# Performance work log

Hardware: AMD Instinct MI355X
Metric: run time of the kernel (lower is better)

The kernel has to match this reference:

```python
import jax, jax.numpy as jnp
import numpy as np

N = 100000      # nodes
E = 3200000     # edges (avg degree 32)
F_IN = 128      # num_node_features
H = 16          # hidden dim (fixed in module)
C = 2           # num_classes


def setup_inputs() -> dict:
    key = jax.random.key(0)
    k0, k1, k2, k3 = jax.random.split(key, 4)
    x = jax.random.normal(k0, (N, F_IN), dtype=jnp.float32)
    edge_index = jax.random.randint(k1, (2, E), 0, N, dtype=jnp.int32)
    # GCNConv params: weight (in,out) + bias (out,) per layer (glorot-ish scale)
    W1 = jax.random.normal(k2, (F_IN, H), dtype=jnp.float32) * (1.0 / np.sqrt(F_IN))
    b1 = jnp.zeros((H,), jnp.float32)
    W2 = jax.random.normal(k3, (H, C), dtype=jnp.float32) * (1.0 / np.sqrt(H))
    b2 = jnp.zeros((C,), jnp.float32)
    return {"x": x, "edge_index": edge_index, "W1": W1, "b1": b1, "W2": W2, "b2": b2}


def _gcn_conv(x, W, b, src, dst, n):
    # GCNConv: h = D^{-1/2}(A+I)D^{-1/2} (x W) + b, with self-loops in src/dst
    h = x @ W                                   # [n, out]
    deg = jax.ops.segment_sum(jnp.ones_like(dst, dtype=h.dtype), dst, num_segments=n)
    dinv = jnp.where(deg > 0, jax.lax.rsqrt(deg), 0.0)
    norm = dinv[src] * dinv[dst]                # [E+n]
    msg = h[src] * norm[:, None]                # gather + scale
    out = jax.ops.segment_sum(msg, dst, num_segments=n)  # scatter-add
    return out + b


def reference(x, edge_index, W1, b1, W2, b2):
    loops = jnp.arange(N, dtype=edge_index.dtype)
    src = jnp.concatenate([edge_index[0], loops])
    dst = jnp.concatenate([edge_index[1], loops])
    h = jax.nn.relu(_gcn_conv(x, W1, b1, src, dst, N))
    # F.dropout(training=False) in eval mode is identity
    out = _gcn_conv(h, W2, b2, src, dst, N)
    return jax.nn.log_softmax(out, axis=1)
```

## Files before the change

### kernel.cpp

```cpp
#include <hip/hip_runtime.h>

#define NN 100000
#define NE 3200000
#define FIN 128
#define HD 16

#define BSH 8
#define BSPAN 256
#define NBKT 391
#define CAP 9216
#define TPB 512

#define FXS 1048576.0f
#define FXI (1.0f / 1048576.0f)

__device__ __forceinline__ float lo2f(unsigned u) {
    union { float f; unsigned i; } v; v.i = u << 16; return v.f;
}
__device__ __forceinline__ float hi2f(unsigned u) {
    union { float f; unsigned i; } v; v.i = u & 0xFFFF0000u; return v.f;
}
__device__ __forceinline__ ushort f2b(float f) {
    union { float f; unsigned u; } v; v.f = f;
    unsigned r = (v.u + 0x7FFFu + ((v.u >> 16) & 1u)) >> 16;
    return (ushort)r;
}
__device__ __forceinline__ unsigned pck(float a, float b) {
    return (unsigned)f2b(a) | ((unsigned)f2b(b) << 16);
}

__global__ __launch_bounds__(TPB) void k_scat(const int* __restrict__ src,
                                              const int* __restrict__ dst,
                                              int* __restrict__ gcnt,
                                              unsigned* __restrict__ csrb) {
    __shared__ int h[NBKT];
    __shared__ int sbuf[TPB];
    __shared__ int lcur[NBKT];
    __shared__ int gbase[NBKT];
    __shared__ unsigned ebuf[8192];
    int b = blockIdx.x, t = threadIdx.x;
    for (int i = t; i < NBKT; i += TPB) h[i] = 0;
    __syncthreads();
    int cq = b * 2048;
    const int4* s4p = (const int4*)src;
    const int4* d4p = (const int4*)dst;
    int4 sv[4], dv[4];
    #pragma unroll
    for (int j = 0; j < 4; ++j) {
        int e4 = cq + j * TPB + t;
        if (e4 < NE / 4) {
            sv[j] = s4p[e4]; dv[j] = d4p[e4];
            atomicAdd(&h[dv[j].x >> BSH], 1);
            atomicAdd(&h[dv[j].y >> BSH], 1);
            atomicAdd(&h[dv[j].z >> BSH], 1);
            atomicAdd(&h[dv[j].w >> BSH], 1);
        }
    }
    __syncthreads();
    sbuf[t] = (t < NBKT) ? h[t] : 0;
    __syncthreads();
    for (int off = 1; off < TPB; off <<= 1) {
        int v = 0;
        if (t >= off) v = sbuf[t - off];
        __syncthreads();
        if (t >= off) sbuf[t] += v;
        __syncthreads();
    }
    if (t < NBKT) {
        int c = h[t];
        int excl = sbuf[t] - c;
        lcur[t] = excl;
        int gb = t * CAP - excl;
        if (c) gb += atomicAdd(&gcnt[t], c);
        gbase[t] = gb;
    }
    __syncthreads();
    #pragma unroll
    for (int j = 0; j < 4; ++j) {
        int e4 = cq + j * TPB + t;
        if (e4 < NE / 4) {
            int bk, p;
            bk = dv[j].x >> BSH; p = atomicAdd(&lcur[bk], 1);
            ebuf[p] = (unsigned)sv[j].x | ((unsigned)(dv[j].x & (BSPAN - 1)) << 17);
            bk = dv[j].y >> BSH; p = atomicAdd(&lcur[bk], 1);
            ebuf[p] = (unsigned)sv[j].y | ((unsigned)(dv[j].y & (BSPAN - 1)) << 17);
            bk = dv[j].z >> BSH; p = atomicAdd(&lcur[bk], 1);
            ebuf[p] = (unsigned)sv[j].z | ((unsigned)(dv[j].z & (BSPAN - 1)) << 17);
            bk = dv[j].w >> BSH; p = atomicAdd(&lcur[bk], 1);
            ebuf[p] = (unsigned)sv[j].w | ((unsigned)(dv[j].w & (BSPAN - 1)) << 17);
        }
    }
    __syncthreads();
    int ecnt = NE - b * 8192; if (ecnt > 8192) ecnt = 8192;
    for (int p = t; p < ecnt; p += TPB) {
        unsigned pl = ebuf[p];
        int lo = 0, hi = NBKT;
        while (lo < hi) { int mid = (lo + hi) >> 1;
                          if (sbuf[mid] > p) hi = mid; else lo = mid + 1; }
        csrb[gbase[lo] + p] = pl;
    }
}

__global__ __launch_bounds__(TPB) void k_gemm1d(const int* __restrict__ gcnt,
                                                const unsigned int* __restrict__ csrb,
                                                const float* __restrict__ x,
                                                const float* __restrict__ W1,
                                                float* __restrict__ dinv,
                                                ushort* __restrict__ h1b) {
    __shared__ float wsm[FIN][HD];
    __shared__ int cnt[BSPAN];
    __shared__ float dvs[BSPAN];
    int b = blockIdx.x, t = threadIdx.x;
    if (t < BSPAN) cnt[t] = 0;
    for (int i = t; i < FIN * HD; i += TPB) wsm[i >> 4][i & 15] = W1[i];
    __syncthreads();
    int e0 = b * CAP, e1 = e0 + gcnt[b];
    for (int e = e0 + t; e < e1; e += TPB) atomicAdd(&cnt[csrb[e] >> 17], 1);
    __syncthreads();
    if (t < BSPAN) {
        int node = b * BSPAN + t;
        float di = rsqrtf((float)cnt[t] + 1.0f);
        dvs[t] = di;
        if (node < NN) dinv[node] = di;
    }
    __syncthreads();
    int loc = t >> 1, half = t & 1;
    int node = b * BSPAN + loc;
    if (node >= NN) return;
    int g = half * 8;
    const float4* xr = (const float4*)(x + (size_t)node * FIN);
    float a0 = 0.f, a1 = 0.f, a2 = 0.f, a3 = 0.f;
    float a4 = 0.f, a5 = 0.f, a6 = 0.f, a7 = 0.f;
    #pragma unroll
    for (int k4 = 0; k4 < FIN / 4; ++k4) {
        float4 v = xr[k4];
        #pragma unroll
        for (int kk = 0; kk < 4; ++kk) {
            float vk = (kk == 0) ? v.x : (kk == 1) ? v.y : (kk == 2) ? v.z : v.w;
            float4 w0 = *(const float4*)&wsm[k4 * 4 + kk][g];
            float4 w1 = *(const float4*)&wsm[k4 * 4 + kk][g + 4];
            a0 += vk * w0.x; a1 += vk * w0.y; a2 += vk * w0.z; a3 += vk * w0.w;
            a4 += vk * w1.x; a5 += vk * w1.y; a6 += vk * w1.z; a7 += vk * w1.w;
        }
    }
    float di = dvs[loc];
    uint4 r = {pck(a0 * di, a1 * di), pck(a2 * di, a3 * di),
               pck(a4 * di, a5 * di), pck(a6 * di, a7 * di)};
    *(uint4*)(h1b + (size_t)node * HD + g) = r;
}

__device__ __forceinline__ void scat16(int* a, uint4 u0, uint4 u1) {
    atomicAdd(a + 0,  __float2int_rn(lo2f(u0.x) * FXS));
    atomicAdd(a + 1,  __float2int_rn(hi2f(u0.x) * FXS));
    atomicAdd(a + 2,  __float2int_rn(lo2f(u0.y) * FXS));
    atomicAdd(a + 3,  __float2int_rn(hi2f(u0.y) * FXS));
    atomicAdd(a + 4,  __float2int_rn(lo2f(u0.z) * FXS));
    atomicAdd(a + 5,  __float2int_rn(hi2f(u0.z) * FXS));
    atomicAdd(a + 6,  __float2int_rn(lo2f(u0.w) * FXS));
    atomicAdd(a + 7,  __float2int_rn(hi2f(u0.w) * FXS));
    atomicAdd(a + 8,  __float2int_rn(lo2f(u1.x) * FXS));
    atomicAdd(a + 9,  __float2int_rn(hi2f(u1.x) * FXS));
    atomicAdd(a + 10, __float2int_rn(lo2f(u1.y) * FXS));
    atomicAdd(a + 11, __float2int_rn(hi2f(u1.y) * FXS));
    atomicAdd(a + 12, __float2int_rn(lo2f(u1.z) * FXS));
    atomicAdd(a + 13, __float2int_rn(hi2f(u1.z) * FXS));
    atomicAdd(a + 14, __float2int_rn(lo2f(u1.w) * FXS));
    atomicAdd(a + 15, __float2int_rn(hi2f(u1.w) * FXS));
}

__global__ __launch_bounds__(TPB) void k_aggs1(const int* __restrict__ gcnt,
                                               const unsigned int* __restrict__ csrb,
                                               const ushort* __restrict__ h1b,
                                               const float* __restrict__ dinv,
                                               const float* __restrict__ b1,
                                               const float* __restrict__ W2,
                                               float* __restrict__ g_s) {
    __shared__ int acc[BSPAN][HD + 1];
    __shared__ float w2s[HD * 2];
    __shared__ float b1s[HD];
    int b = blockIdx.x, t = threadIdx.x;
    for (int i = t; i < BSPAN * (HD + 1); i += TPB) ((int*)acc)[i] = 0;
    if (t < HD * 2) w2s[t] = W2[t];
    else if (t < HD * 3) b1s[t - HD * 2] = b1[t - HD * 2];
    __syncthreads();
    int e0 = b * CAP, e1 = e0 + gcnt[b];
    int e = e0 + t;
    for (; e + TPB < e1; e += 2 * TPB) {
        unsigned pa = csrb[e];
        unsigned pb = csrb[e + TPB];
        const uint4* ra = (const uint4*)(h1b + (size_t)(pa & 0x1FFFF) * HD);
        const uint4* rb = (const uint4*)(h1b + (size_t)(pb & 0x1FFFF) * HD);
        uint4 a0 = ra[0], a1 = ra[1];
        uint4 c0 = rb[0], c1 = rb[1];
        scat16(acc[pa >> 17], a0, a1);
        scat16(acc[pb >> 17], c0, c1);
    }
    if (e < e1) {
        unsigned p = csrb[e];
        const uint4* r = (const uint4*)(h1b + (size_t)(p & 0x1FFFF) * HD);
        uint4 u0 = r[0], u1 = r[1];
        scat16(acc[p >> 17], u0, u1);
    }
    __syncthreads();
    int loc = t >> 1, half = t & 1;
    int node = b * BSPAN + loc;
    if (node < NN) {
        float di = dinv[node];
        const uint4 sv = *(const uint4*)(h1b + (size_t)node * HD + half * 8);
        float sf[8] = {lo2f(sv.x), hi2f(sv.x), lo2f(sv.y), hi2f(sv.y),
                       lo2f(sv.z), hi2f(sv.z), lo2f(sv.w), hi2f(sv.w)};
        const int* a = acc[loc] + half * 8;
        const float* bb = b1s + half * 8;
        const float* ww = w2s + half * 16;
        float p0 = 0.f, p1 = 0.f;
        #pragma unroll
        for (int k = 0; k < 8; ++k) {
            float v = fmaxf(di * ((float)a[k] * FXI + sf[k]) + bb[k], 0.f);
            p0 += v * ww[k * 2];
            p1 += v * ww[k * 2 + 1];
        }
        p0 += __shfl_xor(p0, 1, 64);
        p1 += __shfl_xor(p1, 1, 64);
        if (half == 0) {
            float2 r = {p0 * di, p1 * di};
            *(float2*)(g_s + (size_t)node * 2) = r;
        }
    }
}

__global__ __launch_bounds__(TPB) void k_aggs2(const int* __restrict__ gcnt,
                                               const unsigned int* __restrict__ csrb,
                                               const float* __restrict__ g_s,
                                               const float* __restrict__ dinv,
                                               const float* __restrict__ b2,
                                               float* __restrict__ out) {
    __shared__ int acc[BSPAN * 3];
    int b = blockIdx.x, t = threadIdx.x;
    for (int i = t; i < BSPAN * 3; i += TPB) acc[i] = 0;
    __syncthreads();
    int e0 = b * CAP, e1 = e0 + gcnt[b];
    int e = e0 + t;
    for (; e + TPB < e1; e += 2 * TPB) {
        unsigned pa = csrb[e];
        unsigned pb = csrb[e + TPB];
        float2 va = *(const float2*)(g_s + (size_t)(pa & 0x1FFFF) * 2);
        float2 vb = *(const float2*)(g_s + (size_t)(pb & 0x1FFFF) * 2);
        int la = (pa >> 17) * 3, lb = (pb >> 17) * 3;
        atomicAdd(&acc[la],     __float2int_rn(va.x * FXS));
        atomicAdd(&acc[la + 1], __float2int_rn(va.y * FXS));
        atomicAdd(&acc[lb],     __float2int_rn(vb.x * FXS));
        atomicAdd(&acc[lb + 1], __float2int_rn(vb.y * FXS));
    }
    if (e < e1) {
        unsigned p = csrb[e];
        float2 v = *(const float2*)(g_s + (size_t)(p & 0x1FFFF) * 2);
        int l = (p >> 17) * 3;
        atomicAdd(&acc[l],     __float2int_rn(v.x * FXS));
        atomicAdd(&acc[l + 1], __float2int_rn(v.y * FXS));
    }
    __syncthreads();
    if (t < BSPAN) {
        int node = b * BSPAN + t;
        if (node < NN) {
            float di = dinv[node];
            float2 sv = *(const float2*)(g_s + (size_t)node * 2);
            float o0 = di * ((float)acc[t * 3] * FXI + sv.x) + b2[0];
            float o1 = di * ((float)acc[t * 3 + 1] * FXI + sv.y) + b2[1];
            float mx = fmaxf(o0, o1);
            float l = mx + logf(__expf(o0 - mx) + __expf(o1 - mx));
            float2 r = {o0 - l, o1 - l};
            *(float2*)(out + (size_t)node * 2) = r;
        }
    }
}

extern "C" void kernel_launch(void* const* d_in, const int* in_sizes, int n_in,
                              void* d_out, int out_size, void* d_ws, size_t ws_size,
                              hipStream_t stream) {
    const float* x   = (const float*)d_in[0];
    const int* ei    = (const int*)d_in[1];
    const int* src   = ei;
    const int* dst   = ei + NE;
    const float* W1  = (const float*)d_in[2];
    const float* b1  = (const float*)d_in[3];
    const float* W2  = (const float*)d_in[4];
    const float* b2  = (const float*)d_in[5];
    float* out = (float*)d_out;

    char* w = (char*)d_ws;
    int*   gcnt        = (int*)w;            w += NBKT * 4;
    float* dinv        = (float*)w;          w += NN * 4;
    unsigned int* csrb = (unsigned int*)w;   w += (size_t)NBKT * CAP * 4;
    ushort* h1b        = (ushort*)w;         w += (size_t)NN * HD * 2;
    float* g_s         = (float*)w;          w += NN * 2 * 4;

    hipMemsetAsync(gcnt, 0, NBKT * 4, stream);
    k_scat   <<<NBKT, TPB, 0, stream>>>(src, dst, gcnt, csrb);
    k_gemm1d <<<NBKT, TPB, 0, stream>>>(gcnt, csrb, x, W1, dinv, h1b);
    k_aggs1  <<<NBKT, TPB, 0, stream>>>(gcnt, csrb, h1b, dinv, b1, W2, g_s);
    k_aggs2  <<<NBKT, TPB, 0, stream>>>(gcnt, csrb, g_s, dinv, b2, out);
}
```

Measured before the change: 200.2 us.

## Overlap edge bucketing with X·W1 GEMM in one launch, apply dinv at gather

Merges the edge-scatter kernel and the dense x·W1 projection into one launch, with half the blocks doing each, so the memory-bound GEMM runs alongside the bucketing. Degree normalisation moves into a small separate kernel. The source-side dinv scale is now applied per edge during aggregation, and the stored features are no longer pre-scaled. The aggregation loops are unrolled to four edges per iteration to raise memory-level parallelism. The trade is an extra per-edge dinv gather and one more kernel launch.

```diff
diff --git a/kernel.cpp b/kernel.cpp
--- a/kernel.cpp
+++ b/kernel.cpp
@@ -29,148 +29,149 @@
     return (unsigned)f2b(a) | ((unsigned)f2b(b) << 16);
 }
 
-__global__ __launch_bounds__(TPB) void k_scat(const int* __restrict__ src,
-                                              const int* __restrict__ dst,
-                                              int* __restrict__ gcnt,
-                                              unsigned* __restrict__ csrb) {
-    __shared__ int h[NBKT];
-    __shared__ int sbuf[TPB];
-    __shared__ int lcur[NBKT];
-    __shared__ int gbase[NBKT];
-    __shared__ unsigned ebuf[8192];
-    int b = blockIdx.x, t = threadIdx.x;
-    for (int i = t; i < NBKT; i += TPB) h[i] = 0;
-    __syncthreads();
-    int cq = b * 2048;
-    const int4* s4p = (const int4*)src;
-    const int4* d4p = (const int4*)dst;
-    int4 sv[4], dv[4];
-    #pragma unroll
-    for (int j = 0; j < 4; ++j) {
-        int e4 = cq + j * TPB + t;
-        if (e4 < NE / 4) {
-            sv[j] = s4p[e4]; dv[j] = d4p[e4];
-            atomicAdd(&h[dv[j].x >> BSH], 1);
-            atomicAdd(&h[dv[j].y >> BSH], 1);
-            atomicAdd(&h[dv[j].z >> BSH], 1);
-            atomicAdd(&h[dv[j].w >> BSH], 1);
-        }
-    }
-    __syncthreads();
-    sbuf[t] = (t < NBKT) ? h[t] : 0;
-    __syncthreads();
-    for (int off = 1; off < TPB; off <<= 1) {
-        int v = 0;
-        if (t >= off) v = sbuf[t - off];
-        __syncthreads();
-        if (t >= off) sbuf[t] += v;
-        __syncthreads();
-    }
-    if (t < NBKT) {
-        int c = h[t];
-        int excl = sbuf[t] - c;
-        lcur[t] = excl;
-        int gb = t * CAP - excl;
-        if (c) gb += atomicAdd(&gcnt[t], c);
-        gbase[t] = gb;
-    }
-    __syncthreads();
-    #pragma unroll
-    for (int j = 0; j < 4; ++j) {
-        int e4 = cq + j * TPB + t;
-        if (e4 < NE / 4) {
-            int bk, p;
-            bk = dv[j].x >> BSH; p = atomicAdd(&lcur[bk], 1);
-            ebuf[p] = (unsigned)sv[j].x | ((unsigned)(dv[j].x & (BSPAN - 1)) << 17);
-            bk = dv[j].y >> BSH; p = atomicAdd(&lcur[bk], 1);
-            ebuf[p] = (unsigned)sv[j].y | ((unsigned)(dv[j].y & (BSPAN - 1)) << 17);
-            bk = dv[j].z >> BSH; p = atomicAdd(&lcur[bk], 1);
-            ebuf[p] = (unsigned)sv[j].z | ((unsigned)(dv[j].z & (BSPAN - 1)) << 17);
-            bk = dv[j].w >> BSH; p = atomicAdd(&lcur[bk], 1);
-            ebuf[p] = (unsigned)sv[j].w | ((unsigned)(dv[j].w & (BSPAN - 1)) << 17);
-        }
-    }
-    __syncthreads();
-    int ecnt = NE - b * 8192; if (ecnt > 8192) ecnt = 8192;
-    for (int p = t; p < ecnt; p += TPB) {
-        unsigned pl = ebuf[p];
-        int lo = 0, hi = NBKT;
-        while (lo < hi) { int mid = (lo + hi) >> 1;
-                          if (sbuf[mid] > p) hi = mid; else lo = mid + 1; }
-        csrb[gbase[lo] + p] = pl;
-    }
-}
-
-__global__ __launch_bounds__(TPB) void k_gemm1d(const int* __restrict__ gcnt,
-                                                const unsigned int* __restrict__ csrb,
-                                                const float* __restrict__ x,
-                                                const float* __restrict__ W1,
-                                                float* __restrict__ dinv,
-                                                ushort* __restrict__ h1b) {
-    __shared__ float wsm[FIN][HD];
+union FrontSM {
+    struct { int h[NBKT]; int sbuf[TPB]; int lcur[NBKT]; int gbase[NBKT];
+             unsigned ebuf[8192]; } s;
+    struct { float wsm[FIN][HD]; } g;
+};
+
+__global__ __launch_bounds__(TPB) void k_front(const int* __restrict__ src,
+                                               const int* __restrict__ dst,
+                                               const float* __restrict__ x,
+                                               const float* __restrict__ W1,
+                                               int* __restrict__ gcnt,
+                                               unsigned* __restrict__ csrb,
+                                               ushort* __restrict__ h1u) {
+    __shared__ FrontSM sm;
+    int t = threadIdx.x;
+    if (blockIdx.x < NBKT) {
+        int b = blockIdx.x;
+        for (int i = t; i < NBKT; i += TPB) sm.s.h[i] = 0;
+        __syncthreads();
+        int cq = b * 2048;
+        const int4* s4p = (const int4*)src;
+        const int4* d4p = (const int4*)dst;
+        int4 sv[4], dv[4];
+        #pragma unroll
+        for (int j = 0; j < 4; ++j) {
+            int e4 = cq + j * TPB + t;
+            if (e4 < NE / 4) {
+                sv[j] = s4p[e4]; dv[j] = d4p[e4];
+                atomicAdd(&sm.s.h[dv[j].x >> BSH], 1);
+                atomicAdd(&sm.s.h[dv[j].y >> BSH], 1);
+                atomicAdd(&sm.s.h[dv[j].z >> BSH], 1);
+                atomicAdd(&sm.s.h[dv[j].w >> BSH], 1);
+            }
+        }
+        __syncthreads();
+        sm.s.sbuf[t] = (t < NBKT) ? sm.s.h[t] : 0;
+        __syncthreads();
+        for (int off = 1; off < TPB; off <<= 1) {
+            int v = 0;
+            if (t >= off) v = sm.s.sbuf[t - off];
+            __syncthreads();
+            if (t >= off) sm.s.sbuf[t] += v;
+            __syncthreads();
+        }
+        if (t < NBKT) {
+            int c = sm.s.h[t];
+            int excl = sm.s.sbuf[t] - c;
+            sm.s.lcur[t] = excl;
+            int gb = t * CAP - excl;
+            if (c) gb += atomicAdd(&gcnt[t], c);
+            sm.s.gbase[t] = gb;
+        }
+        __syncthreads();
+        #pragma unroll
+        for (int j = 0; j < 4; ++j) {
+            int e4 = cq + j * TPB + t;
+            if (e4 < NE / 4) {
+                int bk, p;
+                bk = dv[j].x >> BSH; p = atomicAdd(&sm.s.lcur[bk], 1);
+                sm.s.ebuf[p] = (unsigned)sv[j].x | ((unsigned)(dv[j].x & (BSPAN - 1)) << 17);
+                bk = dv[j].y >> BSH; p = atomicAdd(&sm.s.lcur[bk], 1);
+                sm.s.ebuf[p] = (unsigned)sv[j].y | ((unsigned)(dv[j].y & (BSPAN - 1)) << 17);
+                bk = dv[j].z >> BSH; p = atomicAdd(&sm.s.lcur[bk], 1);
+                sm.s.ebuf[p] = (unsigned)sv[j].z | ((unsigned)(dv[j].z & (BSPAN - 1)) << 17);
+                bk = dv[j].w >> BSH; p = atomicAdd(&sm.s.lcur[bk], 1);
+                sm.s.ebuf[p] = (unsigned)sv[j].w | ((unsigned)(dv[j].w & (BSPAN - 1)) << 17);
+            }
+        }
+        __syncthreads();
+        int ecnt = NE - b * 8192; if (ecnt > 8192) ecnt = 8192;
+        for (int p = t; p < ecnt; p += TPB) {
+            unsigned pl = sm.s.ebuf[p];
+            int lo = 0, hi = NBKT;
+            while (lo < hi) { int mid = (lo + hi) >> 1;
+                              if (sm.s.sbuf[mid] > p) hi = mid; else lo = mid + 1; }
+            csrb[sm.s.gbase[lo] + p] = pl;
+        }
+    } else {
+        int b = blockIdx.x - NBKT;
+        for (int i = t; i < FIN * HD; i += TPB) sm.g.wsm[i >> 4][i & 15] = W1[i];
+        __syncthreads();
+        int loc = t >> 1, half = t & 1;
+        int node = b * BSPAN + loc;
+        if (node >= NN) return;
+        int g = half * 8;
+        const float4* xr = (const float4*)(x + (size_t)node * FIN);
+        float a0 = 0.f, a1 = 0.f, a2 = 0.f, a3 = 0.f;
+        float a4 = 0.f, a5 = 0.f, a6 = 0.f, a7 = 0.f;
+        #pragma unroll
+        for (int k4 = 0; k4 < FIN / 4; ++k4) {
+            float4 v = xr[k4];
+            #pragma unroll
+            for (int kk = 0; kk < 4; ++kk) {
+                float vk = (kk == 0) ? v.x : (kk == 1) ? v.y : (kk == 2) ? v.z : v.w;
+                float4 w0 = *(const float4*)&sm.g.wsm[k4 * 4 + kk][g];
+                float4 w1 = *(const float4*)&sm.g.wsm[k4 * 4 + kk][g + 4];
+                a0 += vk * w0.x; a1 += vk * w0.y; a2 += vk * w0.z; a3 += vk * w0.w;
+                a4 += vk * w1.x; a5 += vk * w1.y; a6 += vk * w1.z; a7 += vk * w1.w;
+            }
+        }
+        uint4 r = {pck(a0, a1), pck(a2, a3), pck(a4, a5), pck(a6, a7)};
+        *(uint4*)(h1u + (size_t)node * HD + g) = r;
+    }
+}
+
+__global__ __launch_bounds__(TPB) void k_deg(const int* __restrict__ gcnt,
+                                             const unsigned int* __restrict__ csrb,
+                                             float* __restrict__ dinv) {
     __shared__ int cnt[BSPAN];
-    __shared__ float dvs[BSPAN];
     int b = blockIdx.x, t = threadIdx.x;
     if (t < BSPAN) cnt[t] = 0;
-    for (int i = t; i < FIN * HD; i += TPB) wsm[i >> 4][i & 15] = W1[i];
     __syncthreads();
     int e0 = b * CAP, e1 = e0 + gcnt[b];
     for (int e = e0 + t; e < e1; e += TPB) atomicAdd(&cnt[csrb[e] >> 17], 1);
     __syncthreads();
     if (t < BSPAN) {
         int node = b * BSPAN + t;
-        float di = rsqrtf((float)cnt[t] + 1.0f);
-        dvs[t] = di;
-        if (node < NN) dinv[node] = di;
-    }
-    __syncthreads();
-    int loc = t >> 1, half = t & 1;
-    int node = b * BSPAN + loc;
-    if (node >= NN) return;
-    int g = half * 8;
-    const float4* xr = (const float4*)(x + (size_t)node * FIN);
-    float a0 = 0.f, a1 = 0.f, a2 = 0.f, a3 = 0.f;
-    float a4 = 0.f, a5 = 0.f, a6 = 0.f, a7 = 0.f;
-    #pragma unroll
-    for (int k4 = 0; k4 < FIN / 4; ++k4) {
-        float4 v = xr[k4];
-        #pragma unroll
-        for (int kk = 0; kk < 4; ++kk) {
-            float vk = (kk == 0) ? v.x : (kk == 1) ? v.y : (kk == 2) ? v.z : v.w;
-            float4 w0 = *(const float4*)&wsm[k4 * 4 + kk][g];
-            float4 w1 = *(const float4*)&wsm[k4 * 4 + kk][g + 4];
-            a0 += vk * w0.x; a1 += vk * w0.y; a2 += vk * w0.z; a3 += vk * w0.w;
-            a4 += vk * w1.x; a5 += vk * w1.y; a6 += vk * w1.z; a7 += vk * w1.w;
-        }
-    }
-    float di = dvs[loc];
-    uint4 r = {pck(a0 * di, a1 * di), pck(a2 * di, a3 * di),
-               pck(a4 * di, a5 * di), pck(a6 * di, a7 * di)};
-    *(uint4*)(h1b + (size_t)node * HD + g) = r;
-}
-
-__device__ __forceinline__ void scat16(int* a, uint4 u0, uint4 u1) {
-    atomicAdd(a + 0,  __float2int_rn(lo2f(u0.x) * FXS));
-    atomicAdd(a + 1,  __float2int_rn(hi2f(u0.x) * FXS));
-    atomicAdd(a + 2,  __float2int_rn(lo2f(u0.y) * FXS));
-    atomicAdd(a + 3,  __float2int_rn(hi2f(u0.y) * FXS));
-    atomicAdd(a + 4,  __float2int_rn(lo2f(u0.z) * FXS));
-    atomicAdd(a + 5,  __float2int_rn(hi2f(u0.z) * FXS));
-    atomicAdd(a + 6,  __float2int_rn(lo2f(u0.w) * FXS));
-    atomicAdd(a + 7,  __float2int_rn(hi2f(u0.w) * FXS));
-    atomicAdd(a + 8,  __float2int_rn(lo2f(u1.x) * FXS));
-    atomicAdd(a + 9,  __float2int_rn(hi2f(u1.x) * FXS));
-    atomicAdd(a + 10, __float2int_rn(lo2f(u1.y) * FXS));
-    atomicAdd(a + 11, __float2int_rn(hi2f(u1.y) * FXS));
-    atomicAdd(a + 12, __float2int_rn(lo2f(u1.z) * FXS));
-    atomicAdd(a + 13, __float2int_rn(hi2f(u1.z) * FXS));
-    atomicAdd(a + 14, __float2int_rn(lo2f(u1.w) * FXS));
-    atomicAdd(a + 15, __float2int_rn(hi2f(u1.w) * FXS));
+        if (node < NN) dinv[node] = rsqrtf((float)cnt[t] + 1.0f);
+    }
+}
+
+__device__ __forceinline__ void scat16s(int* a, uint4 u0, uint4 u1, float s) {
+    atomicAdd(a + 0,  __float2int_rn(lo2f(u0.x) * s));
+    atomicAdd(a + 1,  __float2int_rn(hi2f(u0.x) * s));
+    atomicAdd(a + 2,  __float2int_rn(lo2f(u0.y) * s));
+    atomicAdd(a + 3,  __float2int_rn(hi2f(u0.y) * s));
+    atomicAdd(a + 4,  __float2int_rn(lo2f(u0.z) * s));
+    atomicAdd(a + 5,  __float2int_rn(hi2f(u0.z) * s));
+    atomicAdd(a + 6,  __float2int_rn(lo2f(u0.w) * s));
+    atomicAdd(a + 7,  __float2int_rn(hi2f(u0.w) * s));
+    atomicAdd(a + 8,  __float2int_rn(lo2f(u1.x) * s));
+    atomicAdd(a + 9,  __float2int_rn(hi2f(u1.x) * s));
+    atomicAdd(a + 10, __float2int_rn(lo2f(u1.y) * s));
+    atomicAdd(a + 11, __float2int_rn(hi2f(u1.y) * s));
+    atomicAdd(a + 12, __float2int_rn(lo2f(u1.z) * s));
+    atomicAdd(a + 13, __float2int_rn(hi2f(u1.z) * s));
+    atomicAdd(a + 14, __float2int_rn(lo2f(u1.w) * s));
+    atomicAdd(a + 15, __float2int_rn(hi2f(u1.w) * s));
 }
 
 __global__ __launch_bounds__(TPB) void k_aggs1(const int* __restrict__ gcnt,
                                                const unsigned int* __restrict__ csrb,
-                                               const ushort* __restrict__ h1b,
+                                               const ushort* __restrict__ h1u,
                                                const float* __restrict__ dinv,
                                                const float* __restrict__ b1,
                                                const float* __restrict__ W2,
@@ -185,28 +186,39 @@
     __syncthreads();
     int e0 = b * CAP, e1 = e0 + gcnt[b];
     int e = e0 + t;
-    for (; e + TPB < e1; e += 2 * TPB) {
-        unsigned pa = csrb[e];
-        unsigned pb = csrb[e + TPB];
-        const uint4* ra = (const uint4*)(h1b + (size_t)(pa & 0x1FFFF) * HD);
-        const uint4* rb = (const uint4*)(h1b + (size_t)(pb & 0x1FFFF) * HD);
-        uint4 a0 = ra[0], a1 = ra[1];
-        uint4 c0 = rb[0], c1 = rb[1];
-        scat16(acc[pa >> 17], a0, a1);
-        scat16(acc[pb >> 17], c0, c1);
-    }
-    if (e < e1) {
+    for (; e + 3 * TPB < e1; e += 4 * TPB) {
+        unsigned p0 = csrb[e], p1 = csrb[e + TPB];
+        unsigned p2 = csrb[e + 2 * TPB], p3 = csrb[e + 3 * TPB];
+        float s0 = dinv[p0 & 0x1FFFF] * FXS;
+        float s1 = dinv[p1 & 0x1FFFF] * FXS;
+        float s2 = dinv[p2 & 0x1FFFF] * FXS;
+        float s3 = dinv[p3 & 0x1FFFF] * FXS;
+        const uint4* r0 = (const uint4*)(h1u + (size_t)(p0 & 0x1FFFF) * HD);
+        const uint4* r1 = (const uint4*)(h1u + (size_t)(p1 & 0x1FFFF) * HD);
+        const uint4* r2 = (const uint4*)(h1u + (size_t)(p2 & 0x1FFFF) * HD);
+        const uint4* r3 = (const uint4*)(h1u + (size_t)(p3 & 0x1FFFF) * HD);
+        uint4 a0 = r0[0], b0 = r0[1];
+        uint4 a1 = r1[0], b1v = r1[1];
+        uint4 a2 = r2[0], b2v = r2[1];
+        uint4 a3 = r3[0], b3v = r3[1];
+        scat16s(acc[p0 >> 17], a0, b0, s0);
+        scat16s(acc[p1 >> 17], a1, b1v, s1);
+        scat16s(acc[p2 >> 17], a2, b2v, s2);
+        scat16s(acc[p3 >> 17], a3, b3v, s3);
+    }
+    for (; e < e1; e += TPB) {
         unsigned p = csrb[e];
-        const uint4* r = (const uint4*)(h1b + (size_t)(p & 0x1FFFF) * HD);
+        float s = dinv[p & 0x1FFFF] * FXS;
+        const uint4* r = (const uint4*)(h1u + (size_t)(p & 0x1FFFF) * HD);
         uint4 u0 = r[0], u1 = r[1];
-        scat16(acc[p >> 17], u0, u1);
+        scat16s(acc[p >> 17], u0, u1, s);
     }
     __syncthreads();
     int loc = t >> 1, half = t & 1;
     int node = b * BSPAN + loc;
     if (node < NN) {
         float di = dinv[node];
-        const uint4 sv = *(const uint4*)(h1b + (size_t)node * HD + half * 8);
+        const uint4 sv = *(const uint4*)(h1u + (size_t)node * HD + half * 8);
         float sf[8] = {lo2f(sv.x), hi2f(sv.x), lo2f(sv.y), hi2f(sv.y),
                        lo2f(sv.z), hi2f(sv.z), lo2f(sv.w), hi2f(sv.w)};
         const int* a = acc[loc] + half * 8;
@@ -215,7 +227,7 @@
         float p0 = 0.f, p1 = 0.f;
         #pragma unroll
         for (int k = 0; k < 8; ++k) {
-            float v = fmaxf(di * ((float)a[k] * FXI + sf[k]) + bb[k], 0.f);
+            float v = fmaxf(di * ((float)a[k] * FXI + sf[k] * di) + bb[k], 0.f);
             p0 += v * ww[k * 2];
             p1 += v * ww[k * 2 + 1];
         }
@@ -240,18 +252,25 @@
     __syncthreads();
     int e0 = b * CAP, e1 = e0 + gcnt[b];
     int e = e0 + t;
-    for (; e + TPB < e1; e += 2 * TPB) {
-        unsigned pa = csrb[e];
-        unsigned pb = csrb[e + TPB];
-        float2 va = *(const float2*)(g_s + (size_t)(pa & 0x1FFFF) * 2);
-        float2 vb = *(const float2*)(g_s + (size_t)(pb & 0x1FFFF) * 2);
-        int la = (pa >> 17) * 3, lb = (pb >> 17) * 3;
-        atomicAdd(&acc[la],     __float2int_rn(va.x * FXS));
-        atomicAdd(&acc[la + 1], __float2int_rn(va.y * FXS));
-        atomicAdd(&acc[lb],     __float2int_rn(vb.x * FXS));
-        atomicAdd(&acc[lb + 1], __float2int_rn(vb.y * FXS));
-    }
-    if (e < e1) {
+    for (; e + 3 * TPB < e1; e += 4 * TPB) {
+        unsigned p0 = csrb[e], p1 = csrb[e + TPB];
+        unsigned p2 = csrb[e + 2 * TPB], p3 = csrb[e + 3 * TPB];
+        float2 v0 = *(const float2*)(g_s + (size_t)(p0 & 0x1FFFF) * 2);
+        float2 v1 = *(const float2*)(g_s + (size_t)(p1 & 0x1FFFF) * 2);
+        float2 v2 = *(const float2*)(g_s + (size_t)(p2 & 0x1FFFF) * 2);
+        float2 v3 = *(const float2*)(g_s + (size_t)(p3 & 0x1FFFF) * 2);
+        int l0 = (p0 >> 17) * 3, l1 = (p1 >> 17) * 3;
+        int l2 = (p2 >> 17) * 3, l3 = (p3 >> 17) * 3;
+        atomicAdd(&acc[l0],     __float2int_rn(v0.x * FXS));
+        atomicAdd(&acc[l0 + 1], __float2int_rn(v0.y * FXS));
+        atomicAdd(&acc[l1],     __float2int_rn(v1.x * FXS));
+        atomicAdd(&acc[l1 + 1], __float2int_rn(v1.y * FXS));
+        atomicAdd(&acc[l2],     __float2int_rn(v2.x * FXS));
+        atomicAdd(&acc[l2 + 1], __float2int_rn(v2.y * FXS));
+        atomicAdd(&acc[l3],     __float2int_rn(v3.x * FXS));
+        atomicAdd(&acc[l3 + 1], __float2int_rn(v3.y * FXS));
+    }
+    for (; e < e1; e += TPB) {
         unsigned p = csrb[e];
         float2 v = *(const float2*)(g_s + (size_t)(p & 0x1FFFF) * 2);
         int l = (p >> 17) * 3;
@@ -291,12 +310,12 @@
     int*   gcnt        = (int*)w;            w += NBKT * 4;
     float* dinv        = (float*)w;          w += NN * 4;
     unsigned int* csrb = (unsigned int*)w;   w += (size_t)NBKT * CAP * 4;
-    ushort* h1b        = (ushort*)w;         w += (size_t)NN * HD * 2;
+    ushort* h1u        = (ushort*)w;         w += (size_t)NN * HD * 2;
     float* g_s         = (float*)w;          w += NN * 2 * 4;
 
     hipMemsetAsync(gcnt, 0, NBKT * 4, stream);
-    k_scat   <<<NBKT, TPB, 0, stream>>>(src, dst, gcnt, csrb);
-    k_gemm1d <<<NBKT, TPB, 0, stream>>>(gcnt, csrb, x, W1, dinv, h1b);
-    k_aggs1  <<<NBKT, TPB, 0, stream>>>(gcnt, csrb, h1b, dinv, b1, W2, g_s);
-    k_aggs2  <<<NBKT, TPB, 0, stream>>>(gcnt, csrb, g_s, dinv, b2, out);
-}
+    k_front <<<2 * NBKT, TPB, 0, stream>>>(src, dst, x, W1, gcnt, csrb, h1u);
+    k_deg   <<<NBKT, TPB, 0, stream>>>(gcnt, csrb, dinv);
+    k_aggs1 <<<NBKT, TPB, 0, stream>>>(gcnt, csrb, h1u, dinv, b1, W2, g_s);
+    k_aggs2 <<<NBKT, TPB, 0, stream>>>(gcnt, csrb, g_s, dinv, b2, out);
+}
```

After: 209.5 us. 1.05x slower.

## Shrink destination buckets to 64 nodes for more blocks and smaller per-block work

Applied to the files above, without the earlier changes.

Reduces the destination bucket span from 256 to 64 nodes, giving 1563 buckets, and decouples the scatter kernel's edge-chunk count (391 blocks) from the bucket count. The scatter kernel now scans four buckets per thread. The aggregation and GEMM kernels run with 256 threads per block across four times as many blocks, with deeper unrolled gathers. The aim is better load balance and occupancy across CUs, since 391 heavy blocks underfill the GPU. The cost is more scatter-side atomics on gcnt, a longer binary search, and a per-bucket capacity (2600 vs an average of about 2048 edges) that could overflow on skewed graphs.

```diff
diff --git a/kernel.cpp b/kernel.cpp
--- a/kernel.cpp
+++ b/kernel.cpp
@@ -5,11 +5,13 @@
 #define FIN 128
 #define HD 16
 
-#define BSH 8
-#define BSPAN 256
-#define NBKT 391
-#define CAP 9216
+#define BSH 6
+#define BSPAN 64
+#define NBKT 1563
+#define CAP 2600
+#define NCH 391
 #define TPB 512
+#define TPA 256
 
 #define FXS 1048576.0f
 #define FXI (1.0f / 1048576.0f)
@@ -33,13 +35,12 @@
                                               const int* __restrict__ dst,
                                               int* __restrict__ gcnt,
                                               unsigned* __restrict__ csrb) {
-    __shared__ int h[NBKT];
+    __shared__ int pref[NBKT];
+    __shared__ int lcur[NBKT];
     __shared__ int sbuf[TPB];
-    __shared__ int lcur[NBKT];
-    __shared__ int gbase[NBKT];
     __shared__ unsigned ebuf[8192];
     int b = blockIdx.x, t = threadIdx.x;
-    for (int i = t; i < NBKT; i += TPB) h[i] = 0;
+    for (int i = t; i < NBKT; i += TPB) pref[i] = 0;
     __syncthreads();
     int cq = b * 2048;
     const int4* s4p = (const int4*)src;
@@ -50,14 +51,21 @@
         int e4 = cq + j * TPB + t;
         if (e4 < NE / 4) {
             sv[j] = s4p[e4]; dv[j] = d4p[e4];
-            atomicAdd(&h[dv[j].x >> BSH], 1);
-            atomicAdd(&h[dv[j].y >> BSH], 1);
-            atomicAdd(&h[dv[j].z >> BSH], 1);
-            atomicAdd(&h[dv[j].w >> BSH], 1);
-        }
-    }
-    __syncthreads();
-    sbuf[t] = (t < NBKT) ? h[t] : 0;
+            atomicAdd(&pref[dv[j].x >> BSH], 1);
+            atomicAdd(&pref[dv[j].y >> BSH], 1);
+            atomicAdd(&pref[dv[j].z >> BSH], 1);
+            atomicAdd(&pref[dv[j].w >> BSH], 1);
+        }
+    }
+    __syncthreads();
+    int c4[4], base4 = t * 4, s = 0;
+    #pragma unroll
+    for (int i = 0; i < 4; ++i) {
+        int j = base4 + i;
+        c4[i] = (j < NBKT) ? pref[j] : 0;
+        s += c4[i];
+    }
+    sbuf[t] = s;
     __syncthreads();
     for (int off = 1; off < TPB; off <<= 1) {
         int v = 0;
@@ -66,13 +74,15 @@
         if (t >= off) sbuf[t] += v;
         __syncthreads();
     }
-    if (t < NBKT) {
-        int c = h[t];
-        int excl = sbuf[t] - c;
-        lcur[t] = excl;
-        int gb = t * CAP - excl;
-        if (c) gb += atomicAdd(&gcnt[t], c);
-        gbase[t] = gb;
+    int run = sbuf[t] - s;
+    #pragma unroll
+    for (int i = 0; i < 4; ++i) {
+        int j = base4 + i;
+        if (j < NBKT) {
+            lcur[j] = run;
+            run += c4[i];
+            pref[j] = run;
+        }
     }
     __syncthreads();
     #pragma unroll
@@ -91,17 +101,29 @@
         }
     }
     __syncthreads();
+    #pragma unroll
+    for (int i = 0; i < 4; ++i) {
+        int j = base4 + i;
+        if (j < NBKT) {
+            int inc = pref[j];
+            int excl = inc - c4[i];
+            int gb = j * CAP - excl;
+            if (c4[i]) gb += atomicAdd(&gcnt[j], c4[i]);
+            lcur[j] = gb;
+        }
+    }
+    __syncthreads();
     int ecnt = NE - b * 8192; if (ecnt > 8192) ecnt = 8192;
     for (int p = t; p < ecnt; p += TPB) {
         unsigned pl = ebuf[p];
         int lo = 0, hi = NBKT;
         while (lo < hi) { int mid = (lo + hi) >> 1;
-                          if (sbuf[mid] > p) hi = mid; else lo = mid + 1; }
-        csrb[gbase[lo] + p] = pl;
-    }
-}
-
-__global__ __launch_bounds__(TPB) void k_gemm1d(const int* __restrict__ gcnt,
+                          if (pref[mid] > p) hi = mid; else lo = mid + 1; }
+        csrb[lcur[lo] + p] = pl;
+    }
+}
+
+__global__ __launch_bounds__(TPA) void k_gemm1d(const int* __restrict__ gcnt,
                                                 const unsigned int* __restrict__ csrb,
                                                 const float* __restrict__ x,
                                                 const float* __restrict__ W1,
@@ -112,10 +134,10 @@
     __shared__ float dvs[BSPAN];
     int b = blockIdx.x, t = threadIdx.x;
     if (t < BSPAN) cnt[t] = 0;
-    for (int i = t; i < FIN * HD; i += TPB) wsm[i >> 4][i & 15] = W1[i];
+    for (int i = t; i < FIN * HD; i += TPA) wsm[i >> 4][i & 15] = W1[i];
     __syncthreads();
     int e0 = b * CAP, e1 = e0 + gcnt[b];
-    for (int e = e0 + t; e < e1; e += TPB) atomicAdd(&cnt[csrb[e] >> 17], 1);
+    for (int e = e0 + t; e < e1; e += TPA) atomicAdd(&cnt[csrb[e] >> 17], 1);
     __syncthreads();
     if (t < BSPAN) {
         int node = b * BSPAN + t;
@@ -124,29 +146,25 @@
         if (node < NN) dinv[node] = di;
     }
     __syncthreads();
-    int loc = t >> 1, half = t & 1;
+    int loc = t >> 2;
     int node = b * BSPAN + loc;
     if (node >= NN) return;
-    int g = half * 8;
+    int g = (t & 3) * 4;
     const float4* xr = (const float4*)(x + (size_t)node * FIN);
     float a0 = 0.f, a1 = 0.f, a2 = 0.f, a3 = 0.f;
-    float a4 = 0.f, a5 = 0.f, a6 = 0.f, a7 = 0.f;
     #pragma unroll
     for (int k4 = 0; k4 < FIN / 4; ++k4) {
         float4 v = xr[k4];
         #pragma unroll
         for (int kk = 0; kk < 4; ++kk) {
             float vk = (kk == 0) ? v.x : (kk == 1) ? v.y : (kk == 2) ? v.z : v.w;
-            float4 w0 = *(const float4*)&wsm[k4 * 4 + kk][g];
-            float4 w1 = *(const float4*)&wsm[k4 * 4 + kk][g + 4];
-            a0 += vk * w0.x; a1 += vk * w0.y; a2 += vk * w0.z; a3 += vk * w0.w;
-            a4 += vk * w1.x; a5 += vk * w1.y; a6 += vk * w1.z; a7 += vk * w1.w;
+            float4 w = *(const float4*)&wsm[k4 * 4 + kk][g];
+            a0 += vk * w.x; a1 += vk * w.y; a2 += vk * w.z; a3 += vk * w.w;
         }
     }
     float di = dvs[loc];
-    uint4 r = {pck(a0 * di, a1 * di), pck(a2 * di, a3 * di),
-               pck(a4 * di, a5 * di), pck(a6 * di, a7 * di)};
-    *(uint4*)(h1b + (size_t)node * HD + g) = r;
+    ushort4 r = {f2b(a0 * di), f2b(a1 * di), f2b(a2 * di), f2b(a3 * di)};
+    *(ushort4*)(h1b + (size_t)node * HD + g) = r;
 }
 
 __device__ __forceinline__ void scat16(int* a, uint4 u0, uint4 u1) {
@@ -168,7 +186,7 @@
     atomicAdd(a + 15, __float2int_rn(hi2f(u1.w) * FXS));
 }
 
-__global__ __launch_bounds__(TPB) void k_aggs1(const int* __restrict__ gcnt,
+__global__ __launch_bounds__(TPA) void k_aggs1(const int* __restrict__ gcnt,
                                                const unsigned int* __restrict__ csrb,
                                                const ushort* __restrict__ h1b,
                                                const float* __restrict__ dinv,
@@ -179,23 +197,29 @@
     __shared__ float w2s[HD * 2];
     __shared__ float b1s[HD];
     int b = blockIdx.x, t = threadIdx.x;
-    for (int i = t; i < BSPAN * (HD + 1); i += TPB) ((int*)acc)[i] = 0;
+    for (int i = t; i < BSPAN * (HD + 1); i += TPA) ((int*)acc)[i] = 0;
     if (t < HD * 2) w2s[t] = W2[t];
     else if (t < HD * 3) b1s[t - HD * 2] = b1[t - HD * 2];
     __syncthreads();
     int e0 = b * CAP, e1 = e0 + gcnt[b];
     int e = e0 + t;
-    for (; e + TPB < e1; e += 2 * TPB) {
-        unsigned pa = csrb[e];
-        unsigned pb = csrb[e + TPB];
-        const uint4* ra = (const uint4*)(h1b + (size_t)(pa & 0x1FFFF) * HD);
-        const uint4* rb = (const uint4*)(h1b + (size_t)(pb & 0x1FFFF) * HD);
-        uint4 a0 = ra[0], a1 = ra[1];
-        uint4 c0 = rb[0], c1 = rb[1];
-        scat16(acc[pa >> 17], a0, a1);
-        scat16(acc[pb >> 17], c0, c1);
-    }
-    if (e < e1) {
+    for (; e + 3 * TPA < e1; e += 4 * TPA) {
+        unsigned p0 = csrb[e], p1 = csrb[e + TPA];
+        unsigned p2 = csrb[e + 2 * TPA], p3 = csrb[e + 3 * TPA];
+        const uint4* r0 = (const uint4*)(h1b + (size_t)(p0 & 0x1FFFF) * HD);
+        const uint4* r1 = (const uint4*)(h1b + (size_t)(p1 & 0x1FFFF) * HD);
+        const uint4* r2 = (const uint4*)(h1b + (size_t)(p2 & 0x1FFFF) * HD);
+        const uint4* r3 = (const uint4*)(h1b + (size_t)(p3 & 0x1FFFF) * HD);
+        uint4 a0 = r0[0], b0 = r0[1];
+        uint4 a1 = r1[0], b1v = r1[1];
+        uint4 a2 = r2[0], b2v = r2[1];
+        uint4 a3 = r3[0], b3v = r3[1];
+        scat16(acc[p0 >> 17], a0, b0);
+        scat16(acc[p1 >> 17], a1, b1v);
+        scat16(acc[p2 >> 17], a2, b2v);
+        scat16(acc[p3 >> 17], a3, b3v);
+    }
+    for (; e < e1; e += TPA) {
         unsigned p = csrb[e];
         const uint4* r = (const uint4*)(h1b + (size_t)(p & 0x1FFFF) * HD);
         uint4 u0 = r[0], u1 = r[1];
@@ -204,7 +228,7 @@
     __syncthreads();
     int loc = t >> 1, half = t & 1;
     int node = b * BSPAN + loc;
-    if (node < NN) {
+    if (t < 2 * BSPAN && node < NN) {
         float di = dinv[node];
         const uint4 sv = *(const uint4*)(h1b + (size_t)node * HD + half * 8);
         float sf[8] = {lo2f(sv.x), hi2f(sv.x), lo2f(sv.y), hi2f(sv.y),
@@ -228,7 +252,7 @@
     }
 }
 
-__global__ __launch_bounds__(TPB) void k_aggs2(const int* __restrict__ gcnt,
+__global__ __launch_bounds__(TPA) void k_aggs2(const int* __restrict__ gcnt,
                                                const unsigned int* __restrict__ csrb,
                                                const float* __restrict__ g_s,
                                                const float* __restrict__ dinv,
@@ -236,22 +260,29 @@
                                                float* __restrict__ out) {
     __shared__ int acc[BSPAN * 3];
     int b = blockIdx.x, t = threadIdx.x;
-    for (int i = t; i < BSPAN * 3; i += TPB) acc[i] = 0;
+    for (int i = t; i < BSPAN * 3; i += TPA) acc[i] = 0;
     __syncthreads();
     int e0 = b * CAP, e1 = e0 + gcnt[b];
     int e = e0 + t;
-    for (; e + TPB < e1; e += 2 * TPB) {
-        unsigned pa = csrb[e];
-        unsigned pb = csrb[e + TPB];
-        float2 va = *(const float2*)(g_s + (size_t)(pa & 0x1FFFF) * 2);
-        float2 vb = *(const float2*)(g_s + (size_t)(pb & 0x1FFFF) * 2);
-        int la = (pa >> 17) * 3, lb = (pb >> 17) * 3;
-        atomicAdd(&acc[la],     __float2int_rn(va.x * FXS));
-        atomicAdd(&acc[la + 1], __float2int_rn(va.y * FXS));
-        atomicAdd(&acc[lb],     __float2int_rn(vb.x * FXS));
-        atomicAdd(&acc[lb + 1], __float2int_rn(vb.y * FXS));
-    }
-    if (e < e1) {
+    for (; e + 3 * TPA < e1; e += 4 * TPA) {
+        unsigned p0 = csrb[e], p1 = csrb[e + TPA];
+        unsigned p2 = csrb[e + 2 * TPA], p3 = csrb[e + 3 * TPA];
+        float2 v0 = *(const float2*)(g_s + (size_t)(p0 & 0x1FFFF) * 2);
+        float2 v1 = *(const float2*)(g_s + (size_t)(p1 & 0x1FFFF) * 2);
+        float2 v2 = *(const float2*)(g_s + (size_t)(p2 & 0x1FFFF) * 2);
+        float2 v3 = *(const float2*)(g_s + (size_t)(p3 & 0x1FFFF) * 2);
+        int l0 = (p0 >> 17) * 3, l1 = (p1 >> 17) * 3;
+        int l2 = (p2 >> 17) * 3, l3 = (p3 >> 17) * 3;
+        atomicAdd(&acc[l0],     __float2int_rn(v0.x * FXS));
+        atomicAdd(&acc[l0 + 1], __float2int_rn(v0.y * FXS));
+        atomicAdd(&acc[l1],     __float2int_rn(v1.x * FXS));
+        atomicAdd(&acc[l1 + 1], __float2int_rn(v1.y * FXS));
+        atomicAdd(&acc[l2],     __float2int_rn(v2.x * FXS));
+        atomicAdd(&acc[l2 + 1], __float2int_rn(v2.y * FXS));
+        atomicAdd(&acc[l3],     __float2int_rn(v3.x * FXS));
+        atomicAdd(&acc[l3 + 1], __float2int_rn(v3.y * FXS));
+    }
+    for (; e < e1; e += TPA) {
         unsigned p = csrb[e];
         float2 v = *(const float2*)(g_s + (size_t)(p & 0x1FFFF) * 2);
         int l = (p >> 17) * 3;
@@ -295,8 +326,8 @@
     float* g_s         = (float*)w;          w += NN * 2 * 4;
 
     hipMemsetAsync(gcnt, 0, NBKT * 4, stream);
-    k_scat   <<<NBKT, TPB, 0, stream>>>(src, dst, gcnt, csrb);
-    k_gemm1d <<<NBKT, TPB, 0, stream>>>(gcnt, csrb, x, W1, dinv, h1b);
-    k_aggs1  <<<NBKT, TPB, 0, stream>>>(gcnt, csrb, h1b, dinv, b1, W2, g_s);
-    k_aggs2  <<<NBKT, TPB, 0, stream>>>(gcnt, csrb, g_s, dinv, b2, out);
-}
+    k_scat   <<<NCH, TPB, 0, stream>>>(src, dst, gcnt, csrb);
+    k_gemm1d <<<NBKT, TPA, 0, stream>>>(gcnt, csrb, x, W1, dinv, h1b);
+    k_aggs1  <<<NBKT, TPA, 0, stream>>>(gcnt, csrb, h1b, dinv, b1, W2, g_s);
+    k_aggs2  <<<NBKT, TPA, 0, stream>>>(gcnt, csrb, g_s, dinv, b2, out);
+}
```

New measurement: 216.4 us. 8.1% more time.

## Split edge scatter into smaller blocks and unroll gather loops by four

Applied to the files above, without the earlier changes.

The bucket-scatter kernel now runs 782 blocks of 256 threads, each handling 4096 edges instead of 8192. Each thread scans two bucket counts, and the global atomic reservation moves after the local placement so it overlaps less with the scan. The two aggregation kernels unroll their edge loops by four instead of two, putting more gathers in flight per thread. The scatter change aims for better occupancy and more blocks across CUs, at the cost of twice as many global atomics on bucket counters and smaller contiguous writes.

```diff
diff --git a/kernel.cpp b/kernel.cpp
--- a/kernel.cpp
+++ b/kernel.cpp
@@ -9,6 +9,8 @@
 #define BSPAN 256
 #define NBKT 391
 #define CAP 9216
+#define NCHS 782
+#define TPS 256
 #define TPB 512
 
 #define FXS 1048576.0f
@@ -29,25 +31,26 @@
     return (unsigned)f2b(a) | ((unsigned)f2b(b) << 16);
 }
 
-__global__ __launch_bounds__(TPB) void k_scat(const int* __restrict__ src,
+__global__ __launch_bounds__(TPS) void k_scat(const int* __restrict__ src,
                                               const int* __restrict__ dst,
                                               int* __restrict__ gcnt,
                                               unsigned* __restrict__ csrb) {
     __shared__ int h[NBKT];
-    __shared__ int sbuf[TPB];
+    __shared__ int pref[NBKT];
     __shared__ int lcur[NBKT];
     __shared__ int gbase[NBKT];
-    __shared__ unsigned ebuf[8192];
+    __shared__ int sbuf[TPS];
+    __shared__ unsigned ebuf[4096];
     int b = blockIdx.x, t = threadIdx.x;
-    for (int i = t; i < NBKT; i += TPB) h[i] = 0;
-    __syncthreads();
-    int cq = b * 2048;
+    for (int i = t; i < NBKT; i += TPS) h[i] = 0;
+    __syncthreads();
+    int cq = b * 1024;
     const int4* s4p = (const int4*)src;
     const int4* d4p = (const int4*)dst;
     int4 sv[4], dv[4];
     #pragma unroll
     for (int j = 0; j < 4; ++j) {
-        int e4 = cq + j * TPB + t;
+        int e4 = cq + j * TPS + t;
         if (e4 < NE / 4) {
             sv[j] = s4p[e4]; dv[j] = d4p[e4];
             atomicAdd(&h[dv[j].x >> BSH], 1);
@@ -57,27 +60,36 @@
         }
     }
     __syncthreads();
-    sbuf[t] = (t < NBKT) ? h[t] : 0;
-    __syncthreads();
-    for (int off = 1; off < TPB; off <<= 1) {
+    int c2[2], b0 = t * 2, s = 0;
+    #pragma unroll
+    for (int k = 0; k < 2; ++k) {
+        int j = b0 + k;
+        c2[k] = (j < NBKT) ? h[j] : 0;
+        s += c2[k];
+    }
+    sbuf[t] = s;
+    __syncthreads();
+    for (int off = 1; off < TPS; off <<= 1) {
         int v = 0;
         if (t >= off) v = sbuf[t - off];
         __syncthreads();
         if (t >= off) sbuf[t] += v;
         __syncthreads();
     }
-    if (t < NBKT) {
-        int c = h[t];
-        int excl = sbuf[t] - c;
-        lcur[t] = excl;
-        int gb = t * CAP - excl;
-        if (c) gb += atomicAdd(&gcnt[t], c);
-        gbase[t] = gb;
+    int run = sbuf[t] - s;
+    #pragma unroll
+    for (int k = 0; k < 2; ++k) {
+        int j = b0 + k;
+        if (j < NBKT) {
+            lcur[j] = run;
+            run += c2[k];
+            pref[j] = run;
+        }
     }
     __syncthreads();
     #pragma unroll
     for (int j = 0; j < 4; ++j) {
-        int e4 = cq + j * TPB + t;
+        int e4 = cq + j * TPS + t;
         if (e4 < NE / 4) {
             int bk, p;
             bk = dv[j].x >> BSH; p = atomicAdd(&lcur[bk], 1);
@@ -91,12 +103,23 @@
         }
     }
     __syncthreads();
-    int ecnt = NE - b * 8192; if (ecnt > 8192) ecnt = 8192;
-    for (int p = t; p < ecnt; p += TPB) {
+    #pragma unroll
+    for (int k = 0; k < 2; ++k) {
+        int j = b0 + k;
+        if (j < NBKT) {
+            int excl = pref[j] - c2[k];
+            int gb = j * CAP - excl;
+            if (c2[k]) gb += atomicAdd(&gcnt[j], c2[k]);
+            gbase[j] = gb;
+        }
+    }
+    __syncthreads();
+    int ecnt = NE - b * 4096; if (ecnt > 4096) ecnt = 4096;
+    for (int p = t; p < ecnt; p += TPS) {
         unsigned pl = ebuf[p];
         int lo = 0, hi = NBKT;
         while (lo < hi) { int mid = (lo + hi) >> 1;
-                          if (sbuf[mid] > p) hi = mid; else lo = mid + 1; }
+                          if (pref[mid] > p) hi = mid; else lo = mid + 1; }
         csrb[gbase[lo] + p] = pl;
     }
 }
@@ -185,17 +208,23 @@
     __syncthreads();
     int e0 = b * CAP, e1 = e0 + gcnt[b];
     int e = e0 + t;
-    for (; e + TPB < e1; e += 2 * TPB) {
-        unsigned pa = csrb[e];
-        unsigned pb = csrb[e + TPB];
-        const uint4* ra = (const uint4*)(h1b + (size_t)(pa & 0x1FFFF) * HD);
-        const uint4* rb = (const uint4*)(h1b + (size_t)(pb & 0x1FFFF) * HD);
-        uint4 a0 = ra[0], a1 = ra[1];
-        uint4 c0 = rb[0], c1 = rb[1];
-        scat16(acc[pa >> 17], a0, a1);
-        scat16(acc[pb >> 17], c0, c1);
-    }
-    if (e < e1) {
+    for (; e + 3 * TPB < e1; e += 4 * TPB) {
+        unsigned p0 = csrb[e], p1 = csrb[e + TPB];
+        unsigned p2 = csrb[e + 2 * TPB], p3 = csrb[e + 3 * TPB];
+        const uint4* r0 = (const uint4*)(h1b + (size_t)(p0 & 0x1FFFF) * HD);
+        const uint4* r1 = (const uint4*)(h1b + (size_t)(p1 & 0x1FFFF) * HD);
+        const uint4* r2 = (const uint4*)(h1b + (size_t)(p2 & 0x1FFFF) * HD);
+        const uint4* r3 = (const uint4*)(h1b + (size_t)(p3 & 0x1FFFF) * HD);
+        uint4 a0 = r0[0], b0 = r0[1];
+        uint4 a1 = r1[0], b1v = r1[1];
+        uint4 a2 = r2[0], b2v = r2[1];
+        uint4 a3 = r3[0], b3v = r3[1];
+        scat16(acc[p0 >> 17], a0, b0);
+        scat16(acc[p1 >> 17], a1, b1v);
+        scat16(acc[p2 >> 17], a2, b2v);
+        scat16(acc[p3 >> 17], a3, b3v);
+    }
+    for (; e < e1; e += TPB) {
         unsigned p = csrb[e];
         const uint4* r = (const uint4*)(h1b + (size_t)(p & 0x1FFFF) * HD);
         uint4 u0 = r[0], u1 = r[1];
@@ -240,18 +269,25 @@
     __syncthreads();
     int e0 = b * CAP, e1 = e0 + gcnt[b];
     int e = e0 + t;
-    for (; e + TPB < e1; e += 2 * TPB) {
-        unsigned pa = csrb[e];
-        unsigned pb = csrb[e + TPB];
-        float2 va = *(const float2*)(g_s + (size_t)(pa & 0x1FFFF) * 2);
-        float2 vb = *(const float2*)(g_s + (size_t)(pb & 0x1FFFF) * 2);
-        int la = (pa >> 17) * 3, lb = (pb >> 17) * 3;
-        atomicAdd(&acc[la],     __float2int_rn(va.x * FXS));
-        atomicAdd(&acc[la + 1], __float2int_rn(va.y * FXS));
-        atomicAdd(&acc[lb],     __float2int_rn(vb.x * FXS));
-        atomicAdd(&acc[lb + 1], __float2int_rn(vb.y * FXS));
-    }
-    if (e < e1) {
+    for (; e + 3 * TPB < e1; e += 4 * TPB) {
+        unsigned p0 = csrb[e], p1 = csrb[e + TPB];
+        unsigned p2 = csrb[e + 2 * TPB], p3 = csrb[e + 3 * TPB];
+        float2 v0 = *(const float2*)(g_s + (size_t)(p0 & 0x1FFFF) * 2);
+        float2 v1 = *(const float2*)(g_s + (size_t)(p1 & 0x1FFFF) * 2);
+        float2 v2 = *(const float2*)(g_s + (size_t)(p2 & 0x1FFFF) * 2);
+        float2 v3 = *(const float2*)(g_s + (size_t)(p3 & 0x1FFFF) * 2);
+        int l0 = (p0 >> 17) * 3, l1 = (p1 >> 17) * 3;
+        int l2 = (p2 >> 17) * 3, l3 = (p3 >> 17) * 3;
+        atomicAdd(&acc[l0],     __float2int_rn(v0.x * FXS));
+        atomicAdd(&acc[l0 + 1], __float2int_rn(v0.y * FXS));
+        atomicAdd(&acc[l1],     __float2int_rn(v1.x * FXS));
+        atomicAdd(&acc[l1 + 1], __float2int_rn(v1.y * FXS));
+        atomicAdd(&acc[l2],     __float2int_rn(v2.x * FXS));
+        atomicAdd(&acc[l2 + 1], __float2int_rn(v2.y * FXS));
+        atomicAdd(&acc[l3],     __float2int_rn(v3.x * FXS));
+        atomicAdd(&acc[l3 + 1], __float2int_rn(v3.y * FXS));
+    }
+    for (; e < e1; e += TPB) {
         unsigned p = csrb[e];
         float2 v = *(const float2*)(g_s + (size_t)(p & 0x1FFFF) * 2);
         int l = (p >> 17) * 3;
@@ -295,7 +331,7 @@
     float* g_s         = (float*)w;          w += NN * 2 * 4;
 
     hipMemsetAsync(gcnt, 0, NBKT * 4, stream);
-    k_scat   <<<NBKT, TPB, 0, stream>>>(src, dst, gcnt, csrb);
+    k_scat   <<<NCHS, TPS, 0, stream>>>(src, dst, gcnt, csrb);
     k_gemm1d <<<NBKT, TPB, 0, stream>>>(gcnt, csrb, x, W1, dinv, h1b);
     k_aggs1  <<<NBKT, TPB, 0, stream>>>(gcnt, csrb, h1b, dinv, b1, W2, g_s);
     k_aggs2  <<<NBKT, TPB, 0, stream>>>(gcnt, csrb, g_s, dinv, b2, out);
```

Result: slower. 222.2 us (+11.0%).
